# Kernel tuning notes

Hardware: AMD Instinct MI355X
Metric: run time of the kernel (lower is better)

Reference implementation:

```python
import jax, jax.numpy as jnp
import numpy as np


def setup_inputs() -> dict:
    key = jax.random.key(0)
    B, D, KD, TR, NI = 4096, 512, 448, 64, 16  # batch, d_model, key_dim_size, t_resolution, num_iters
    DK = KD + TR                                # full query/key width = 512
    ks = jax.random.split(key, 9)

    def w(k, fan_in, fan_out):
        return jax.random.normal(k, (fan_in, fan_out), jnp.float32) / jnp.sqrt(jnp.float32(fan_in))

    return {
        "x":   jax.random.normal(ks[0], (B, D), jnp.float32),
        "Wik": w(ks[1], D, KD),        # input_key_proj
        "Wiv": w(ks[2], D, D),         # input_value_proj (value dim = d_model)
        "Wq":  w(ks[3], D, DK),        # query_proj
        "Wk":  w(ks[4], D + TR, DK),   # key_proj on concat(block_out, sin(t*t_enc))
        "Wv":  w(ks[5], D, D),         # value_proj
        "W1":  w(ks[6], D, D),         # block MLP layer 1
        "W2":  w(ks[7], D, D),         # block MLP layer 2
        "t_emb": 0.02 * jax.random.normal(ks[8], (NI + 1, D), jnp.float32),  # block time conditioning
    }


def reference(x, Wik, Wiv, Wq, Wk, Wv, W1, W2, t_emb):
    B, D = x.shape
    DK = Wq.shape[1]
    TR = Wk.shape[0] - D           # t_resolution
    NI = t_emb.shape[0] - 1        # num_iters
    dt = x.dtype
    scale = jnp.asarray(1.0 / np.sqrt(DK), dt)
    # t_encoding = pi * (1/2)**i
    t_enc = jnp.pi * (0.5 ** jnp.arange(TR, dtype=dt))

    def attend(q, K, V, n):  # q:[B,DK], K:[B,NI,DK], V:[B,NI,D]; n static valid length
        s = jnp.einsum('bd,btd->bt', q, K[:, :n]) * scale
        p = jax.nn.softmax(s, axis=-1)
        return jnp.einsum('bt,btd->bd', p, V[:, :n])

    def block(A, t):  # opaque self.block(A, t=t): MLP with per-t conditioning
        return jax.nn.gelu(A @ W1 + t_emb[t]) @ W2

    # preallocated growing KV cache (in-place append instead of concat)
    K = jnp.zeros((B, NI, DK), dt)
    V = jnp.zeros((B, NI, D), dt)
    k0 = jnp.pad(x @ Wik, ((0, 0), (0, TR)))  # initial key padded to DK (sin(0)=0 encoding)
    K = K.at[:, 0].set(k0)
    V = V.at[:, 0].set(x @ Wiv)
    q = jnp.ones((B, DK), dt)

    for t in range(NI - 1):  # static unrolled recurrence over iterations
        A = attend(q, K, V, t + 1)
        Bt = block(A, t)
        sin_t = jnp.broadcast_to(jnp.sin(t * t_enc), (B, TR))
        K = K.at[:, t + 1].set(jnp.concatenate([Bt, sin_t], axis=-1) @ Wk)
        V = V.at[:, t + 1].set(Bt @ Wv)
        q = Bt @ Wq

    A = attend(q, K, V, NI)
    return block(A, NI)  # final block call with t = num_iters
```

## Files before the change

kernel.cpp:

```cpp
#include <hip/hip_runtime.h>
#include <hip/hip_bf16.h>
#include <math.h>

typedef unsigned short u16;
using bf16x8 = __attribute__((ext_vector_type(8))) short;
using f32x4  = __attribute__((ext_vector_type(4))) float;

__device__ inline float b2f(u16 u) {
  unsigned v = ((unsigned)u) << 16;
  return __builtin_bit_cast(float, v);
}
__device__ inline u16 f2b(float f) {
  unsigned u = __builtin_bit_cast(unsigned, f);
  u += 0x7fffu + ((u >> 16) & 1u);
  return (u16)(u >> 16);
}
__device__ inline float gelu_f(float x) {
  float x3 = x * x * x;
  return 0.5f * x * (1.f + tanhf(0.7978845608028654f * (x + 0.044715f * x3)));
}
__device__ inline void gload_lds16(const void* g, void* lds) {
  __builtin_amdgcn_global_load_lds((const __attribute__((address_space(1))) void*)g,
                                   (__attribute__((address_space(3))) void*)lds,
                                   16, 0, 0);
}

#define EPI_SPLIT2 0
#define EPI_F32    1
#define EPI_INIT2H 2

template<int EPI>
__global__ __launch_bounds__(256)
void gemm64(const u16* __restrict__ Aptr, int lda,
            const u16* __restrict__ BT,
            void* __restrict__ out0, void* __restrict__ out1, void* __restrict__ out2,
            const u16* __restrict__ fvec, const float* __restrict__ tembv, int t1)
{
  constexpr int BM = 128, BN = 64, WN = 32, NR = 2, MR = 4;
  __shared__ alignas(16) char Ash[3][BM * 128];
  __shared__ alignas(16) char Bsh[3][BN * 128];
  const int tid = threadIdx.x, lane = tid & 63, wid = tid >> 6;
  const int wm = wid >> 1, wn = wid & 1;
  const int bm = blockIdx.x, bn = blockIdx.y;

  const int rIn = lane >> 3;
  const int c16log = (lane & 7) ^ (rIn & 7);

  auto stage = [&](int buf, int kt) {
    #pragma unroll
    for (int i = 0; i < 4; ++i) {
      int c = wid * 4 + i;
      int row = c * 8 + rIn;
      gload_lds16(Aptr + (size_t)(bm * BM + row) * lda + kt + c16log * 8,
                  Ash[buf] + c * 1024);
    }
    #pragma unroll
    for (int i = 0; i < 2; ++i) {
      int c = wid * 2 + i;
      int row = c * 8 + rIn;
      gload_lds16(BT + (size_t)(bn * BN + row) * 512 + kt + c16log * 8,
                  Bsh[buf] + c * 1024);
    }
  };

  f32x4 acc[MR][NR] = {};
  stage(0, 0);
  stage(1, 64);
  #pragma unroll
  for (int kt = 0; kt < 8; ++kt) {
    const int cb = kt % 3;
    if (kt < 6) {
      stage((kt + 2) % 3, (kt + 2) * 64);
      asm volatile("s_waitcnt vmcnt(12)" ::: "memory");
    } else if (kt == 6) {
      asm volatile("s_waitcnt vmcnt(6)" ::: "memory");
    } else {
      asm volatile("s_waitcnt vmcnt(0)" ::: "memory");
    }
    __builtin_amdgcn_s_barrier();
    asm volatile("" ::: "memory");
    #pragma unroll
    for (int kk = 0; kk < 64; kk += 32) {
      bf16x8 af[MR], bfr[NR];
      #pragma unroll
      for (int m = 0; m < MR; ++m) {
        int R = wm * 64 + m * 16 + (lane & 15);
        int c16 = (kk >> 3) + (lane >> 4);
        af[m] = *(const bf16x8*)(Ash[cb] + R * 128 + ((c16 ^ (R & 7)) << 4));
      }
      #pragma unroll
      for (int n = 0; n < NR; ++n) {
        int R = wn * WN + n * 16 + (lane & 15);
        int c16 = (kk >> 3) + (lane >> 4);
        bfr[n] = *(const bf16x8*)(Bsh[cb] + R * 128 + ((c16 ^ (R & 7)) << 4));
      }
      #pragma unroll
      for (int m = 0; m < MR; ++m)
        #pragma unroll
        for (int n = 0; n < NR; ++n)
          acc[m][n] = __builtin_amdgcn_mfma_f32_16x16x32_bf16(af[m], bfr[n], acc[m][n], 0, 0, 0);
    }
    asm volatile("" ::: "memory");
    __builtin_amdgcn_s_barrier();
    asm volatile("" ::: "memory");
  }

  const int row0 = bm * BM + wm * 64;
  const int col0 = bn * BN + wn * WN;
  #pragma unroll
  for (int m = 0; m < MR; ++m) {
    #pragma unroll
    for (int n = 0; n < NR; ++n) {
      #pragma unroll
      for (int i = 0; i < 4; ++i) {
        int row = row0 + m * 16 + (lane >> 4) * 4 + i;
        int col = col0 + n * 16 + (lane & 15);
        float v = acc[m][n][i];
        if constexpr (EPI == EPI_SPLIT2) {
          if (col < 512) {
            ((u16*)out0)[((size_t)row * 16 + t1) * 512 + col] = f2b(v + b2f(fvec[col]));
          } else {
            ((u16*)out1)[((size_t)row * 16 + t1) * 512 + (col - 512)] = f2b(v);
          }
        } else if constexpr (EPI == EPI_INIT2H) {
          if (col < 512) {
            ((u16*)out0)[(size_t)row * 16 * 512 + col] = f2b(v);
          } else {
            ((u16*)out1)[(size_t)row * 16 * 512 + (col - 512)] = f2b(v);
            ((u16*)out2)[(size_t)row * 512 + (col - 512)] =
                f2b(gelu_f(v + tembv[col - 512]));
          }
        } else {
          ((float*)out0)[(size_t)row * 512 + col] = v;
        }
      }
    }
  }
}

struct BatchJobs {
  const u16* A[5];
  const u16* BT[5];
  u16* O[5];
  int M[5];
};

__global__ __launch_bounds__(256)
void gemm_batch(BatchJobs jb)
{
  constexpr int BM = 128, BN = 64, WN = 32, NR = 2, MR = 4;
  const int z = blockIdx.z;
  if ((int)blockIdx.x * BM >= jb.M[z]) return;
  const u16* __restrict__ Aptr = jb.A[z];
  const u16* __restrict__ BT   = jb.BT[z];
  u16* __restrict__ Optr       = jb.O[z];

  __shared__ alignas(16) char Ash[3][BM * 128];
  __shared__ alignas(16) char Bsh[3][BN * 128];
  const int tid = threadIdx.x, lane = tid & 63, wid = tid >> 6;
  const int wm = wid >> 1, wn = wid & 1;
  const int bm = blockIdx.x, bn = blockIdx.y;

  const int rIn = lane >> 3;
  const int c16log = (lane & 7) ^ (rIn & 7);

  auto stage = [&](int buf, int kt) {
    #pragma unroll
    for (int i = 0; i < 4; ++i) {
      int c = wid * 4 + i;
      int row = c * 8 + rIn;
      gload_lds16(Aptr + (size_t)(bm * BM + row) * 512 + kt + c16log * 8,
                  Ash[buf] + c * 1024);
    }
    #pragma unroll
    for (int i = 0; i < 2; ++i) {
      int c = wid * 2 + i;
      int row = c * 8 + rIn;
      gload_lds16(BT + (size_t)(bn * BN + row) * 512 + kt + c16log * 8,
                  Bsh[buf] + c * 1024);
    }
  };

  f32x4 acc[MR][NR] = {};
  stage(0, 0);
  stage(1, 64);
  #pragma unroll
  for (int kt = 0; kt < 8; ++kt) {
    const int cb = kt % 3;
    if (kt < 6) {
      stage((kt + 2) % 3, (kt + 2) * 64);
      asm volatile("s_waitcnt vmcnt(12)" ::: "memory");
    } else if (kt == 6) {
      asm volatile("s_waitcnt vmcnt(6)" ::: "memory");
    } else {
      asm volatile("s_waitcnt vmcnt(0)" ::: "memory");
    }
    __builtin_amdgcn_s_barrier();
    asm volatile("" ::: "memory");
    #pragma unroll
    for (int kk = 0; kk < 64; kk += 32) {
      bf16x8 af[MR], bfr[NR];
      #pragma unroll
      for (int m = 0; m < MR; ++m) {
        int R = wm * 64 + m * 16 + (lane & 15);
        int c16 = (kk >> 3) + (lane >> 4);
        af[m] = *(const bf16x8*)(Ash[cb] + R * 128 + ((c16 ^ (R & 7)) << 4));
      }
      #pragma unroll
      for (int n = 0; n < NR; ++n) {
        int R = wn * WN + n * 16 + (lane & 15);
        int c16 = (kk >> 3) + (lane >> 4);
        bfr[n] = *(const bf16x8*)(Bsh[cb] + R * 128 + ((c16 ^ (R & 7)) << 4));
      }
      #pragma unroll
      for (int m = 0; m < MR; ++m)
        #pragma unroll
        for (int n = 0; n < NR; ++n)
          acc[m][n] = __builtin_amdgcn_mfma_f32_16x16x32_bf16(af[m], bfr[n], acc[m][n], 0, 0, 0);
    }
    asm volatile("" ::: "memory");
    __builtin_amdgcn_s_barrier();
    asm volatile("" ::: "memory");
  }

  const int row0 = bm * BM + wm * 64;
  const int col0 = bn * BN + wn * WN;
  #pragma unroll
  for (int m = 0; m < MR; ++m)
    #pragma unroll
    for (int n = 0; n < NR; ++n)
      #pragma unroll
      for (int i = 0; i < 4; ++i) {
        int row = row0 + m * 16 + (lane >> 4) * 4 + i;
        int col = col0 + n * 16 + (lane & 15);
        Optr[(size_t)row * 512 + col] = f2b(acc[m][n][i]);
      }
}

__global__ __launch_bounds__(256)
void attend_kernel(const u16* __restrict__ qv, const u16* __restrict__ Kc,
                   const u16* __restrict__ VWc, u16* __restrict__ Hout,
                   const float* __restrict__ temb, int n)
{
  const int lane = threadIdx.x & 63;
  const int w = threadIdx.x >> 6;
  const int b = blockIdx.x * 4 + w;
  const float scale = 0.04419417382415922f;
  const size_t base = (size_t)b * 512 + lane * 8;
  bf16x8 q8 = *(const bf16x8*)(qv + base);
  float qf[8];
  #pragma unroll
  for (int j = 0; j < 8; ++j) qf[j] = b2f((u16)q8[j]);
  float s[16];
  float mx = -1e30f;
  #pragma unroll
  for (int t = 0; t < 16; ++t) {
    if (t < n) {
      bf16x8 k8 = *(const bf16x8*)(Kc + ((size_t)b * 16 + t) * 512 + lane * 8);
      float d = 0.f;
      #pragma unroll
      for (int j = 0; j < 8; ++j) d += qf[j] * b2f((u16)k8[j]);
      #pragma unroll
      for (int off = 32; off > 0; off >>= 1) d += __shfl_xor(d, off, 64);
      s[t] = d * scale;
      mx = fmaxf(mx, s[t]);
    }
  }
  float p[16], sum = 0.f;
  #pragma unroll
  for (int t = 0; t < 16; ++t) if (t < n) { p[t] = expf(s[t] - mx); sum += p[t]; }
  const float inv = 1.f / sum;
  float a[8] = {};
  #pragma unroll
  for (int t = 0; t < 16; ++t) {
    if (t < n) {
      bf16x8 v8 = *(const bf16x8*)(VWc + ((size_t)b * 16 + t) * 512 + lane * 8);
      float pt = p[t] * inv;
      #pragma unroll
      for (int j = 0; j < 8; ++j) a[j] += pt * b2f((u16)v8[j]);
    }
  }
  bf16x8 o;
  #pragma unroll
  for (int j = 0; j < 8; ++j)
    o[j] = (short)f2b(gelu_f(a[j] + temb[lane * 8 + j]));
  *(bf16x8*)(Hout + base) = o;
}

__global__ __launch_bounds__(256)
void prep_kernel(const float* __restrict__ x,   const float* __restrict__ Wik,
                 const float* __restrict__ Wiv, const float* __restrict__ Wq,
                 const float* __restrict__ Wk,  const float* __restrict__ Wv,
                 const float* __restrict__ W1,  const float* __restrict__ W2,
                 u16* __restrict__ W1T, u16* __restrict__ W2T, u16* __restrict__ WqT,
                 u16* __restrict__ WkT, u16* __restrict__ WvT,
                 u16* __restrict__ W2b, u16* __restrict__ Wivb, u16* __restrict__ xb,
                 u16* __restrict__ Wikpadb, u16* __restrict__ biasKpad)
{
  const int bid = blockIdx.x, tid = threadIdx.x;
  if (bid < 1280) {
    __shared__ float tile[32][33];
    const int mat = bid >> 8, local = bid & 255;
    const float* in = (mat == 0) ? W1 : (mat == 1) ? W2 : (mat == 2) ? Wq
                    : (mat == 3) ? Wk : Wv;
    u16* out = (mat == 0) ? W1T : (mat == 1) ? W2T : (mat == 2) ? WqT
             : (mat == 3) ? WkT : WvT;
    const int tx = tid & 31, ty = tid >> 5;
    const int c0 = (local & 15) * 32, r0 = (local >> 4) * 32;
    #pragma unroll
    for (int rr = 0; rr < 32; rr += 8)
      tile[ty + rr][tx] = in[(size_t)(r0 + ty + rr) * 512 + c0 + tx];
    __syncthreads();
    #pragma unroll
    for (int rr = 0; rr < 32; rr += 8)
      out[(size_t)(c0 + ty + rr) * 512 + r0 + tx] = f2b(tile[tx][ty + rr]);
  } else if (bid < 3840) {
    const float* in; u16* out; int local;
    if (bid < 1536)      { in = W2;  out = W2b;  local = bid - 1280; }
    else if (bid < 1792) { in = Wiv; out = Wivb; local = bid - 1536; }
    else                 { in = x;   out = xb;   local = bid - 1792; }
    const int i = local * 256 + tid;
    const float4 v = ((const float4*)in)[i];
    ushort4 o;
    o.x = f2b(v.x); o.y = f2b(v.y); o.z = f2b(v.z); o.w = f2b(v.w);
    ((ushort4*)out)[i] = o;
  } else if (bid < 4096) {
    const int local = bid - 3840;
    const int e = local * 1024 + tid * 4;
    const int r = e >> 9, c0 = e & 511;
    ushort4 o;
    float v0 = (c0 + 0 < 448) ? Wik[(size_t)r * 448 + c0 + 0] : 0.f;
    float v1 = (c0 + 1 < 448) ? Wik[(size_t)r * 448 + c0 + 1] : 0.f;
    float v2 = (c0 + 2 < 448) ? Wik[(size_t)r * 448 + c0 + 2] : 0.f;
    float v3 = (c0 + 3 < 448) ? Wik[(size_t)r * 448 + c0 + 3] : 0.f;
    o.x = f2b(v0); o.y = f2b(v1); o.z = f2b(v2); o.w = f2b(v3);
    *(ushort4*)(Wikpadb + (size_t)r * 512 + c0) = o;
  } else {
    const int local = bid - 4096;
    const int t = local >> 1;
    const int col = ((local & 1) << 8) + tid;
    float acc = 0.f;
    if (t < 15) {
      #pragma unroll
      for (int r = 0; r < 64; ++r) {
        float tenc = 3.14159265358979323846f * exp2f(-(float)r);
        acc += sinf((float)t * tenc) * Wk[(size_t)(512 + r) * 512 + col];
      }
    }
    biasKpad[(size_t)t * 512 + col] = f2b(acc);
  }
}

extern "C" void kernel_launch(void* const* d_in, const int* in_sizes, int n_in,
                              void* d_out, int out_size, void* d_ws, size_t ws_size,
                              hipStream_t stream)
{
  const float* x    = (const float*)d_in[0];
  const float* Wik  = (const float*)d_in[1];
  const float* Wiv  = (const float*)d_in[2];
  const float* Wq   = (const float*)d_in[3];
  const float* Wk   = (const float*)d_in[4];
  const float* Wv   = (const float*)d_in[5];
  const float* W1   = (const float*)d_in[6];
  const float* W2   = (const float*)d_in[7];
  const float* temb = (const float*)d_in[8];

  char* ws = (char*)d_ws;
  size_t off = 0;
  auto alloc = [&](size_t bytes) {
    char* p = ws + off;
    off += (bytes + 255) & ~(size_t)255;
    return p;
  };
  const size_t SQ = (size_t)512 * 512 * 2;
  u16* W1T     = (u16*)alloc(SQ);
  u16* W2T     = (u16*)alloc(SQ);
  u16* WqT     = (u16*)alloc(SQ);
  u16* WkT     = (u16*)alloc(SQ);
  u16* WvT     = (u16*)alloc(SQ);
  u16* W2b     = (u16*)alloc(SQ);
  u16* Wivb    = (u16*)alloc(SQ);
  u16* Wikpadb = (u16*)alloc(SQ);
  u16* biasKpad= (u16*)alloc((size_t)128 * 512 * 2);
  u16* W2Wq    = (u16*)alloc(SQ);
  u16* W2WkD   = (u16*)alloc(SQ);
  u16* W2Wv    = (u16*)alloc(SQ);
  u16* biasC   = (u16*)alloc((size_t)128 * 512 * 2);
  u16* PT2     = (u16*)alloc((size_t)1024 * 512 * 2);
  u16* ITn     = (u16*)alloc((size_t)1024 * 512 * 2);
  u16* xb      = (u16*)alloc((size_t)4096 * 512 * 2);
  u16* Kc      = (u16*)alloc((size_t)4096 * 16 * 512 * 2);
  u16* VWc     = (u16*)alloc((size_t)4096 * 16 * 512 * 2);
  u16* Hb      = (u16*)alloc((size_t)4096 * 512 * 2);

  dim3 blk(256);
  prep_kernel<<<dim3(4352), blk, 0, stream>>>(
      x, Wik, Wiv, Wq, Wk, Wv, W1, W2,
      W1T, W2T, WqT, WkT, WvT, W2b, Wivb, xb, Wikpadb, biasKpad);

  BatchJobs b1 = {};
  b1.A[0] = W2b; b1.BT[0] = WqT; b1.O[0] = W2Wq;  b1.M[0] = 512;
  b1.A[1] = W2b; b1.BT[1] = WkT; b1.O[1] = W2WkD; b1.M[1] = 512;
  b1.A[2] = W2b; b1.BT[2] = WvT; b1.O[2] = W2Wv;  b1.M[2] = 512;
  gemm_batch<<<dim3(4, 8, 3), blk, 0, stream>>>(b1);

  BatchJobs b2 = {};
  b2.A[0] = W2Wq;     b2.BT[0] = W2WkD;   b2.O[0] = PT2;                       b2.M[0] = 512;
  b2.A[1] = W1T;      b2.BT[1] = W2Wv;    b2.O[1] = PT2 + (size_t)512 * 512;   b2.M[1] = 512;
  b2.A[2] = W2Wq;     b2.BT[2] = Wikpadb; b2.O[2] = ITn;                       b2.M[2] = 512;
  b2.A[3] = W1T;      b2.BT[3] = Wivb;    b2.O[3] = ITn + (size_t)512 * 512;   b2.M[3] = 512;
  b2.A[4] = biasKpad; b2.BT[4] = W2Wq;    b2.O[4] = biasC;                     b2.M[4] = 128;
  gemm_batch<<<dim3(4, 8, 5), blk, 0, stream>>>(b2);

  gemm64<EPI_INIT2H><<<dim3(32, 16), blk, 0, stream>>>(
      xb, 512, ITn, Kc, VWc, Hb, nullptr, temb, 0);

  for (int t = 0; t < 15; ++t) {
    gemm64<EPI_SPLIT2><<<dim3(32, 16), blk, 0, stream>>>(
        Hb, 512, PT2, Kc, VWc, nullptr, biasC + (size_t)t * 512, nullptr, t + 1);
    const int ti = (t == 14) ? 16 : t + 1;
    attend_kernel<<<dim3(1024), blk, 0, stream>>>(
        Hb, Kc, VWc, Hb, temb + (size_t)ti * 512, t + 2);
  }
  gemm64<EPI_F32><<<dim3(32, 8), blk, 0, stream>>>(
      Hb, 512, W2T, d_out, nullptr, nullptr, nullptr, nullptr, 0);
}
```

Measured before the change: 518.7 us.

## Fuse recurrence into one persistent kernel with per-block rows held in LDS

Replaces the 32 per-iteration GEMM and attention launches with a single persistent kernel. Each block owns 16 batch rows, keeps its H tile in LDS, and alternates a GEMM phase and an attention phase separated by block barriers, so no kernel relaunches and no global H round-trips are needed. The GEMM phase reads the weight matrix directly from global/L2 into registers for every block without LDS reuse. That greatly raises cache traffic and leaves only one 4-wave block per CU, which trades launch and sync overhead for lower data reuse and occupancy.

```diff
diff --git a/kernel.cpp b/kernel.cpp
--- a/kernel.cpp
+++ b/kernel.cpp
@@ -25,18 +25,166 @@
                                    16, 0, 0);
 }
 
-#define EPI_SPLIT2 0
-#define EPI_F32    1
-#define EPI_INIT2H 2
-
-template<int EPI>
+
+template<int COLS, int F32OUT>
+__device__ __forceinline__ void gemm_phase(
+    const u16* Hs, const u16* __restrict__ BT, const u16* __restrict__ bias,
+    u16* __restrict__ Kc, u16* __restrict__ VWc, float* __restrict__ outp,
+    int r0, int slot, int lane, int wid)
+{
+  bf16x8 areg[16];
+  {
+    const int r = lane & 15, hi = lane >> 4;
+    #pragma unroll
+    for (int kk = 0; kk < 16; ++kk) {
+      const int c16 = (kk * 4 + hi) ^ (r & 7);
+      areg[kk] = *(const bf16x8*)((const char*)Hs + r * 1024 + c16 * 16);
+    }
+  }
+  constexpr int NCT = COLS / 64;
+  const int colb = wid * (COLS / 4);
+  const int rowb = (lane >> 4) * 4;
+  const int hi = lane >> 4;
+
+  auto loadB = [&](bf16x8* dst, int ct) {
+    const u16* base = BT + (size_t)(colb + ct * 16 + (lane & 15)) * 512 + hi * 8;
+    #pragma unroll
+    for (int kk = 0; kk < 16; ++kk)
+      dst[kk] = *(const bf16x8*)(base + kk * 32);
+  };
+  auto epi = [&](int ct, const f32x4& a) {
+    #pragma unroll
+    for (int i = 0; i < 4; ++i) {
+      const int g = colb + ct * 16 + (lane & 15);
+      const int row = r0 + rowb + i;
+      const float v = a[i];
+      if constexpr (F32OUT) {
+        outp[(size_t)row * 512 + g] = v;
+      } else {
+        if (g < 512) {
+          Kc[((size_t)row * 16 + slot) * 512 + g] = f2b(v + b2f(bias[g]));
+        } else {
+          VWc[((size_t)row * 16 + slot) * 512 + (g - 512)] = f2b(v);
+        }
+      }
+    }
+  };
+
+  bf16x8 b0[16], b1[16];
+  #pragma unroll
+  for (int cp = 0; cp < NCT / 2; ++cp) {
+    loadB(b0, 2 * cp);
+    loadB(b1, 2 * cp + 1);
+    f32x4 a0 = {0.f, 0.f, 0.f, 0.f}, a1 = {0.f, 0.f, 0.f, 0.f};
+    #pragma unroll
+    for (int kk = 0; kk < 16; ++kk) {
+      a0 = __builtin_amdgcn_mfma_f32_16x16x32_bf16(areg[kk], b0[kk], a0, 0, 0, 0);
+      a1 = __builtin_amdgcn_mfma_f32_16x16x32_bf16(areg[kk], b1[kk], a1, 0, 0, 0);
+    }
+    epi(2 * cp, a0);
+    epi(2 * cp + 1, a1);
+  }
+}
+
+__global__ __launch_bounds__(256, 1)
+void persist_kernel(const u16* __restrict__ xb,
+                    const u16* __restrict__ ITn, const u16* __restrict__ PT2,
+                    const u16* __restrict__ W2T, const u16* __restrict__ biasC,
+                    const float* __restrict__ temb,
+                    u16* __restrict__ Kc, u16* __restrict__ VWc,
+                    float* __restrict__ outp)
+{
+  __shared__ alignas(16) u16 Hs[16 * 512];
+  const int tid = threadIdx.x, lane = tid & 63, wid = tid >> 6;
+  const int r0 = blockIdx.x * 16;
+  const float scale = 0.04419417382415922f;
+
+  #pragma unroll
+  for (int p = 0; p < 4; ++p) {
+    const int s16 = (p * 4 + wid) * 64 + lane;
+    const int r = s16 >> 6, c16 = s16 & 63;
+    gload_lds16(xb + (size_t)(r0 + r) * 512 + (size_t)(c16 ^ (r & 7)) * 8,
+                (char*)Hs + (size_t)(p * 4 + wid) * 1024);
+  }
+  asm volatile("s_waitcnt vmcnt(0)" ::: "memory");
+  __syncthreads();
+
+  for (int t = -1; t < 15; ++t) {
+    gemm_phase<1024, 0>(Hs, (t == -1) ? ITn : PT2,
+                        biasC + (size_t)((t == -1) ? 15 : t) * 512,
+                        Kc, VWc, nullptr, r0, t + 1, lane, wid);
+    __syncthreads();
+
+    const int n = t + 2;
+    const float* tv = temb + (size_t)((t == 14) ? 16 : t + 1) * 512;
+    for (int rr = 0; rr < 4; ++rr) {
+      const int r = wid * 4 + rr;
+      const bf16x8 q8 = *(const bf16x8*)((const char*)Hs + r * 1024 +
+                                         ((lane ^ (r & 7)) << 4));
+      float qf[8];
+      #pragma unroll
+      for (int j = 0; j < 8; ++j) qf[j] = b2f((u16)q8[j]);
+      const u16* kbase = Kc + ((size_t)(r0 + r) * 16) * 512 + lane * 8;
+      const u16* vbase = VWc + ((size_t)(r0 + r) * 16) * 512 + lane * 8;
+      float s[16];
+      float mx = -1e30f;
+      #pragma unroll
+      for (int j = 0; j < 16; ++j) {
+        if (j < n) {
+          const bf16x8 k8 = *(const bf16x8*)(kbase + j * 512);
+          float d = 0.f;
+          #pragma unroll
+          for (int e = 0; e < 8; ++e) d += qf[e] * b2f((u16)k8[e]);
+          #pragma unroll
+          for (int off = 32; off > 0; off >>= 1) d += __shfl_xor(d, off, 64);
+          s[j] = d * scale;
+          mx = fmaxf(mx, s[j]);
+        }
+      }
+      float p[16], sum = 0.f;
+      #pragma unroll
+      for (int j = 0; j < 16; ++j)
+        if (j < n) { p[j] = expf(s[j] - mx); sum += p[j]; }
+      const float inv = 1.f / sum;
+      float a[8] = {};
+      #pragma unroll
+      for (int j = 0; j < 16; ++j) {
+        if (j < n) {
+          const bf16x8 v8 = *(const bf16x8*)(vbase + j * 512);
+          const float pj = p[j] * inv;
+          #pragma unroll
+          for (int e = 0; e < 8; ++e) a[e] += pj * b2f((u16)v8[e]);
+        }
+      }
+      bf16x8 o;
+      #pragma unroll
+      for (int e = 0; e < 8; ++e)
+        o[e] = (short)f2b(gelu_f(a[e] + tv[lane * 8 + e]));
+      *(bf16x8*)((char*)Hs + r * 1024 + ((lane ^ (r & 7)) << 4)) = o;
+    }
+    __syncthreads();
+  }
+
+  gemm_phase<512, 1>(Hs, W2T, nullptr, nullptr, nullptr, outp, r0, 0, lane, wid);
+}
+
+struct BatchJobs {
+  const u16* A[5];
+  const u16* BT[5];
+  u16* O[5];
+  int M[5];
+};
+
 __global__ __launch_bounds__(256)
-void gemm64(const u16* __restrict__ Aptr, int lda,
-            const u16* __restrict__ BT,
-            void* __restrict__ out0, void* __restrict__ out1, void* __restrict__ out2,
-            const u16* __restrict__ fvec, const float* __restrict__ tembv, int t1)
+void gemm_batch(BatchJobs jb)
 {
   constexpr int BM = 128, BN = 64, WN = 32, NR = 2, MR = 4;
+  const int z = blockIdx.z;
+  if ((int)blockIdx.x * BM >= jb.M[z]) return;
+  const u16* __restrict__ Aptr = jb.A[z];
+  const u16* __restrict__ BT   = jb.BT[z];
+  u16* __restrict__ Optr       = jb.O[z];
+
   __shared__ alignas(16) char Ash[3][BM * 128];
   __shared__ alignas(16) char Bsh[3][BN * 128];
   const int tid = threadIdx.x, lane = tid & 63, wid = tid >> 6;
@@ -51,7 +199,7 @@
     for (int i = 0; i < 4; ++i) {
       int c = wid * 4 + i;
       int row = c * 8 + rIn;
-      gload_lds16(Aptr + (size_t)(bm * BM + row) * lda + kt + c16log * 8,
+      gload_lds16(Aptr + (size_t)(bm * BM + row) * 512 + kt + c16log * 8,
                   Ash[buf] + c * 1024);
     }
     #pragma unroll
@@ -108,124 +256,6 @@
   const int row0 = bm * BM + wm * 64;
   const int col0 = bn * BN + wn * WN;
   #pragma unroll
-  for (int m = 0; m < MR; ++m) {
-    #pragma unroll
-    for (int n = 0; n < NR; ++n) {
-      #pragma unroll
-      for (int i = 0; i < 4; ++i) {
-        int row = row0 + m * 16 + (lane >> 4) * 4 + i;
-        int col = col0 + n * 16 + (lane & 15);
-        float v = acc[m][n][i];
-        if constexpr (EPI == EPI_SPLIT2) {
-          if (col < 512) {
-            ((u16*)out0)[((size_t)row * 16 + t1) * 512 + col] = f2b(v + b2f(fvec[col]));
-          } else {
-            ((u16*)out1)[((size_t)row * 16 + t1) * 512 + (col - 512)] = f2b(v);
-          }
-        } else if constexpr (EPI == EPI_INIT2H) {
-          if (col < 512) {
-            ((u16*)out0)[(size_t)row * 16 * 512 + col] = f2b(v);
-          } else {
-            ((u16*)out1)[(size_t)row * 16 * 512 + (col - 512)] = f2b(v);
-            ((u16*)out2)[(size_t)row * 512 + (col - 512)] =
-                f2b(gelu_f(v + tembv[col - 512]));
-          }
-        } else {
-          ((float*)out0)[(size_t)row * 512 + col] = v;
-        }
-      }
-    }
-  }
-}
-
-struct BatchJobs {
-  const u16* A[5];
-  const u16* BT[5];
-  u16* O[5];
-  int M[5];
-};
-
-__global__ __launch_bounds__(256)
-void gemm_batch(BatchJobs jb)
-{
-  constexpr int BM = 128, BN = 64, WN = 32, NR = 2, MR = 4;
-  const int z = blockIdx.z;
-  if ((int)blockIdx.x * BM >= jb.M[z]) return;
-  const u16* __restrict__ Aptr = jb.A[z];
-  const u16* __restrict__ BT   = jb.BT[z];
-  u16* __restrict__ Optr       = jb.O[z];
-
-  __shared__ alignas(16) char Ash[3][BM * 128];
-  __shared__ alignas(16) char Bsh[3][BN * 128];
-  const int tid = threadIdx.x, lane = tid & 63, wid = tid >> 6;
-  const int wm = wid >> 1, wn = wid & 1;
-  const int bm = blockIdx.x, bn = blockIdx.y;
-
-  const int rIn = lane >> 3;
-  const int c16log = (lane & 7) ^ (rIn & 7);
-
-  auto stage = [&](int buf, int kt) {
-    #pragma unroll
-    for (int i = 0; i < 4; ++i) {
-      int c = wid * 4 + i;
-      int row = c * 8 + rIn;
-      gload_lds16(Aptr + (size_t)(bm * BM + row) * 512 + kt + c16log * 8,
-                  Ash[buf] + c * 1024);
-    }
-    #pragma unroll
-    for (int i = 0; i < 2; ++i) {
-      int c = wid * 2 + i;
-      int row = c * 8 + rIn;
-      gload_lds16(BT + (size_t)(bn * BN + row) * 512 + kt + c16log * 8,
-                  Bsh[buf] + c * 1024);
-    }
-  };
-
-  f32x4 acc[MR][NR] = {};
-  stage(0, 0);
-  stage(1, 64);
-  #pragma unroll
-  for (int kt = 0; kt < 8; ++kt) {
-    const int cb = kt % 3;
-    if (kt < 6) {
-      stage((kt + 2) % 3, (kt + 2) * 64);
-      asm volatile("s_waitcnt vmcnt(12)" ::: "memory");
-    } else if (kt == 6) {
-      asm volatile("s_waitcnt vmcnt(6)" ::: "memory");
-    } else {
-      asm volatile("s_waitcnt vmcnt(0)" ::: "memory");
-    }
-    __builtin_amdgcn_s_barrier();
-    asm volatile("" ::: "memory");
-    #pragma unroll
-    for (int kk = 0; kk < 64; kk += 32) {
-      bf16x8 af[MR], bfr[NR];
-      #pragma unroll
-      for (int m = 0; m < MR; ++m) {
-        int R = wm * 64 + m * 16 + (lane & 15);
-        int c16 = (kk >> 3) + (lane >> 4);
-        af[m] = *(const bf16x8*)(Ash[cb] + R * 128 + ((c16 ^ (R & 7)) << 4));
-      }
-      #pragma unroll
-      for (int n = 0; n < NR; ++n) {
-        int R = wn * WN + n * 16 + (lane & 15);
-        int c16 = (kk >> 3) + (lane >> 4);
-        bfr[n] = *(const bf16x8*)(Bsh[cb] + R * 128 + ((c16 ^ (R & 7)) << 4));
-      }
-      #pragma unroll
-      for (int m = 0; m < MR; ++m)
-        #pragma unroll
-        for (int n = 0; n < NR; ++n)
-          acc[m][n] = __builtin_amdgcn_mfma_f32_16x16x32_bf16(af[m], bfr[n], acc[m][n], 0, 0, 0);
-    }
-    asm volatile("" ::: "memory");
-    __builtin_amdgcn_s_barrier();
-    asm volatile("" ::: "memory");
-  }
-
-  const int row0 = bm * BM + wm * 64;
-  const int col0 = bn * BN + wn * WN;
-  #pragma unroll
   for (int m = 0; m < MR; ++m)
     #pragma unroll
     for (int n = 0; n < NR; ++n)
@@ -235,56 +265,6 @@
         int col = col0 + n * 16 + (lane & 15);
         Optr[(size_t)row * 512 + col] = f2b(acc[m][n][i]);
       }
-}
-
-__global__ __launch_bounds__(256)
-void attend_kernel(const u16* __restrict__ qv, const u16* __restrict__ Kc,
-                   const u16* __restrict__ VWc, u16* __restrict__ Hout,
-                   const float* __restrict__ temb, int n)
-{
-  const int lane = threadIdx.x & 63;
-  const int w = threadIdx.x >> 6;
-  const int b = blockIdx.x * 4 + w;
-  const float scale = 0.04419417382415922f;
-  const size_t base = (size_t)b * 512 + lane * 8;
-  bf16x8 q8 = *(const bf16x8*)(qv + base);
-  float qf[8];
-  #pragma unroll
-  for (int j = 0; j < 8; ++j) qf[j] = b2f((u16)q8[j]);
-  float s[16];
-  float mx = -1e30f;
-  #pragma unroll
-  for (int t = 0; t < 16; ++t) {
-    if (t < n) {
-      bf16x8 k8 = *(const bf16x8*)(Kc + ((size_t)b * 16 + t) * 512 + lane * 8);
-      float d = 0.f;
-      #pragma unroll
-      for (int j = 0; j < 8; ++j) d += qf[j] * b2f((u16)k8[j]);
-      #pragma unroll
-      for (int off = 32; off > 0; off >>= 1) d += __shfl_xor(d, off, 64);
-      s[t] = d * scale;
-      mx = fmaxf(mx, s[t]);
-    }
-  }
-  float p[16], sum = 0.f;
-  #pragma unroll
-  for (int t = 0; t < 16; ++t) if (t < n) { p[t] = expf(s[t] - mx); sum += p[t]; }
-  const float inv = 1.f / sum;
-  float a[8] = {};
-  #pragma unroll
-  for (int t = 0; t < 16; ++t) {
-    if (t < n) {
-      bf16x8 v8 = *(const bf16x8*)(VWc + ((size_t)b * 16 + t) * 512 + lane * 8);
-      float pt = p[t] * inv;
-      #pragma unroll
-      for (int j = 0; j < 8; ++j) a[j] += pt * b2f((u16)v8[j]);
-    }
-  }
-  bf16x8 o;
-  #pragma unroll
-  for (int j = 0; j < 8; ++j)
-    o[j] = (short)f2b(gelu_f(a[j] + temb[lane * 8 + j]));
-  *(bf16x8*)(Hout + base) = o;
 }
 
 __global__ __launch_bounds__(256)
@@ -391,7 +371,6 @@
   u16* xb      = (u16*)alloc((size_t)4096 * 512 * 2);
   u16* Kc      = (u16*)alloc((size_t)4096 * 16 * 512 * 2);
   u16* VWc     = (u16*)alloc((size_t)4096 * 16 * 512 * 2);
-  u16* Hb      = (u16*)alloc((size_t)4096 * 512 * 2);
 
   dim3 blk(256);
   prep_kernel<<<dim3(4352), blk, 0, stream>>>(
@@ -412,16 +391,6 @@
   b2.A[4] = biasKpad; b2.BT[4] = W2Wq;    b2.O[4] = biasC;                     b2.M[4] = 128;
   gemm_batch<<<dim3(4, 8, 5), blk, 0, stream>>>(b2);
 
-  gemm64<EPI_INIT2H><<<dim3(32, 16), blk, 0, stream>>>(
-      xb, 512, ITn, Kc, VWc, Hb, nullptr, temb, 0);
-
-  for (int t = 0; t < 15; ++t) {
-    gemm64<EPI_SPLIT2><<<dim3(32, 16), blk, 0, stream>>>(
-        Hb, 512, PT2, Kc, VWc, nullptr, biasC + (size_t)t * 512, nullptr, t + 1);
-    const int ti = (t == 14) ? 16 : t + 1;
-    attend_kernel<<<dim3(1024), blk, 0, stream>>>(
-        Hb, Kc, VWc, Hb, temb + (size_t)ti * 512, t + 2);
-  }
-  gemm64<EPI_F32><<<dim3(32, 8), blk, 0, stream>>>(
-      Hb, 512, W2T, d_out, nullptr, nullptr, nullptr, nullptr, 0);
-}
+  persist_kernel<<<dim3(256), blk, 0, stream>>>(
+      xb, ITn, PT2, W2T, biasC, temb, Kc, VWc, (float*)d_out);
+}
```

Result: slower. 1.130 ms (+117.9%).

## Fuse recurrence into one persistent cooperative kernel with grid barriers

Applied to the files above, without the earlier changes.

Replaces the 32 separate launches (initial GEMM, 15 GEMM+attend pairs, final GEMM) with a single cooperative persistent kernel of 512 blocks. Software grid barriers built on atomics separate the GEMM and attention phases. The initial step now reuses the split GEMM epilogue and a length-1 attention in place of the special init epilogue. The aim is to remove per-launch overhead and tail gaps between kernels. In exchange it adds barrier spin costs and depends on two blocks fitting per CU, and it falls back to the old launch sequence if the cooperative launch fails.

```diff
diff --git a/kernel.cpp b/kernel.cpp
--- a/kernel.cpp
+++ b/kernel.cpp
@@ -30,19 +30,15 @@
 #define EPI_INIT2H 2
 
 template<int EPI>
-__global__ __launch_bounds__(256)
-void gemm64(const u16* __restrict__ Aptr, int lda,
-            const u16* __restrict__ BT,
-            void* __restrict__ out0, void* __restrict__ out1, void* __restrict__ out2,
-            const u16* __restrict__ fvec, const float* __restrict__ tembv, int t1)
-{
-  constexpr int BM = 128, BN = 64, WN = 32, NR = 2, MR = 4;
-  __shared__ alignas(16) char Ash[3][BM * 128];
-  __shared__ alignas(16) char Bsh[3][BN * 128];
-  const int tid = threadIdx.x, lane = tid & 63, wid = tid >> 6;
+__device__ __forceinline__ void gemm_dev(
+    char* AshB, char* BshB,
+    const u16* __restrict__ Aptr, int lda, const u16* __restrict__ BT,
+    void* __restrict__ out0, void* __restrict__ out1, void* __restrict__ out2,
+    const u16* __restrict__ fvec, const float* __restrict__ tembv,
+    int t1, int bm, int bn, int lane, int wid)
+{
+  constexpr int WN = 32, NR = 2, MR = 4;
   const int wm = wid >> 1, wn = wid & 1;
-  const int bm = blockIdx.x, bn = blockIdx.y;
-
   const int rIn = lane >> 3;
   const int c16log = (lane & 7) ^ (rIn & 7);
 
@@ -51,15 +47,15 @@
     for (int i = 0; i < 4; ++i) {
       int c = wid * 4 + i;
       int row = c * 8 + rIn;
-      gload_lds16(Aptr + (size_t)(bm * BM + row) * lda + kt + c16log * 8,
-                  Ash[buf] + c * 1024);
+      gload_lds16(Aptr + (size_t)(bm * 128 + row) * lda + kt + c16log * 8,
+                  AshB + buf * 16384 + c * 1024);
     }
     #pragma unroll
     for (int i = 0; i < 2; ++i) {
       int c = wid * 2 + i;
       int row = c * 8 + rIn;
-      gload_lds16(BT + (size_t)(bn * BN + row) * 512 + kt + c16log * 8,
-                  Bsh[buf] + c * 1024);
+      gload_lds16(BT + (size_t)(bn * 64 + row) * 512 + kt + c16log * 8,
+                  BshB + buf * 8192 + c * 1024);
     }
   };
 
@@ -86,13 +82,13 @@
       for (int m = 0; m < MR; ++m) {
         int R = wm * 64 + m * 16 + (lane & 15);
         int c16 = (kk >> 3) + (lane >> 4);
-        af[m] = *(const bf16x8*)(Ash[cb] + R * 128 + ((c16 ^ (R & 7)) << 4));
+        af[m] = *(const bf16x8*)(AshB + cb * 16384 + R * 128 + ((c16 ^ (R & 7)) << 4));
       }
       #pragma unroll
       for (int n = 0; n < NR; ++n) {
         int R = wn * WN + n * 16 + (lane & 15);
         int c16 = (kk >> 3) + (lane >> 4);
-        bfr[n] = *(const bf16x8*)(Bsh[cb] + R * 128 + ((c16 ^ (R & 7)) << 4));
+        bfr[n] = *(const bf16x8*)(BshB + cb * 8192 + R * 128 + ((c16 ^ (R & 7)) << 4));
       }
       #pragma unroll
       for (int m = 0; m < MR; ++m)
@@ -105,8 +101,8 @@
     asm volatile("" ::: "memory");
   }
 
-  const int row0 = bm * BM + wm * 64;
-  const int col0 = bn * BN + wn * WN;
+  const int row0 = bm * 128 + wm * 64;
+  const int col0 = bn * 64 + wn * WN;
   #pragma unroll
   for (int m = 0; m < MR; ++m) {
     #pragma unroll
@@ -138,6 +134,127 @@
   }
 }
 
+template<int EPI>
+__global__ __launch_bounds__(256)
+void gemm64(const u16* __restrict__ Aptr, int lda,
+            const u16* __restrict__ BT,
+            void* __restrict__ out0, void* __restrict__ out1, void* __restrict__ out2,
+            const u16* __restrict__ fvec, const float* __restrict__ tembv, int t1)
+{
+  __shared__ alignas(16) char Ash[3 * 16384];
+  __shared__ alignas(16) char Bsh[3 * 8192];
+  gemm_dev<EPI>(Ash, Bsh, Aptr, lda, BT, out0, out1, out2, fvec, tembv, t1,
+                blockIdx.x, blockIdx.y, threadIdx.x & 63, threadIdx.x >> 6);
+}
+
+__device__ __forceinline__ void attend_row(
+    const u16* __restrict__ Hq, const u16* __restrict__ Kc,
+    const u16* __restrict__ VWc, u16* __restrict__ Hout,
+    const float* __restrict__ tv, int n, int r, int lane)
+{
+  const float scale = 0.04419417382415922f;
+  const size_t base = (size_t)r * 512 + lane * 8;
+  bf16x8 q8 = *(const bf16x8*)(Hq + base);
+  float qf[8];
+  #pragma unroll
+  for (int j = 0; j < 8; ++j) qf[j] = b2f((u16)q8[j]);
+  const u16* kbase = Kc + ((size_t)r * 16) * 512 + lane * 8;
+  const u16* vbase = VWc + ((size_t)r * 16) * 512 + lane * 8;
+  float s[16];
+  float mx = -1e30f;
+  #pragma unroll
+  for (int j = 0; j < 16; ++j) {
+    if (j < n) {
+      const bf16x8 k8 = *(const bf16x8*)(kbase + j * 512);
+      float d = 0.f;
+      #pragma unroll
+      for (int e = 0; e < 8; ++e) d += qf[e] * b2f((u16)k8[e]);
+      #pragma unroll
+      for (int off = 32; off > 0; off >>= 1) d += __shfl_xor(d, off, 64);
+      s[j] = d * scale;
+      mx = fmaxf(mx, s[j]);
+    }
+  }
+  float p[16], sum = 0.f;
+  #pragma unroll
+  for (int j = 0; j < 16; ++j)
+    if (j < n) { p[j] = expf(s[j] - mx); sum += p[j]; }
+  const float inv = 1.f / sum;
+  float a[8] = {};
+  #pragma unroll
+  for (int j = 0; j < 16; ++j) {
+    if (j < n) {
+      const bf16x8 v8 = *(const bf16x8*)(vbase + j * 512);
+      const float pj = p[j] * inv;
+      #pragma unroll
+      for (int e = 0; e < 8; ++e) a[e] += pj * b2f((u16)v8[e]);
+    }
+  }
+  bf16x8 o;
+  #pragma unroll
+  for (int e = 0; e < 8; ++e)
+    o[e] = (short)f2b(gelu_f(a[e] + tv[lane * 8 + e]));
+  *(bf16x8*)(Hout + base) = o;
+}
+
+__global__ __launch_bounds__(256)
+void attend_kernel(const u16* __restrict__ qv, const u16* __restrict__ Kc,
+                   const u16* __restrict__ VWc, u16* __restrict__ Hout,
+                   const float* __restrict__ temb, int n)
+{
+  const int lane = threadIdx.x & 63;
+  const int r = blockIdx.x * 4 + (threadIdx.x >> 6);
+  attend_row(qv, Kc, VWc, Hout, temb, n, r, lane);
+}
+
+__device__ __forceinline__ void gridbar(unsigned* bar, unsigned target) {
+  __syncthreads();
+  if (threadIdx.x == 0) {
+    __hip_atomic_fetch_add(bar, 1u, __ATOMIC_RELEASE, __HIP_MEMORY_SCOPE_AGENT);
+    while (__hip_atomic_load(bar, __ATOMIC_RELAXED, __HIP_MEMORY_SCOPE_AGENT) < target)
+      __builtin_amdgcn_s_sleep(8);
+    (void)__hip_atomic_load(bar, __ATOMIC_ACQUIRE, __HIP_MEMORY_SCOPE_AGENT);
+  }
+  __syncthreads();
+}
+
+__global__ __launch_bounds__(256, 2)
+void persist_kernel(const u16* __restrict__ xb,
+                    const u16* __restrict__ ITn, const u16* __restrict__ PT2,
+                    const u16* __restrict__ W2T, const u16* __restrict__ biasC,
+                    const float* __restrict__ temb,
+                    u16* __restrict__ Kc, u16* __restrict__ VWc,
+                    u16* __restrict__ Hb, float* __restrict__ outp,
+                    unsigned* __restrict__ bar)
+{
+  __shared__ alignas(16) char Ash[3 * 16384];
+  __shared__ alignas(16) char Bsh[3 * 8192];
+  const int tid = threadIdx.x, lane = tid & 63, wid = tid >> 6;
+  const int bid = blockIdx.x;
+  unsigned phase = 0;
+
+  for (int t = -1; t < 15; ++t) {
+    gemm_dev<EPI_SPLIT2>(Ash, Bsh,
+                         (t == -1) ? xb : Hb, 512,
+                         (t == -1) ? ITn : PT2,
+                         Kc, VWc, nullptr,
+                         biasC + (size_t)((t == -1) ? 15 : t) * 512, nullptr,
+                         t + 1, bid >> 4, bid & 15, lane, wid);
+    gridbar(bar, 512u * (++phase));
+
+    const int n = t + 2;
+    const float* tv = temb + (size_t)((t == 14) ? 16 : t + 1) * 512;
+    #pragma unroll
+    for (int rr = 0; rr < 2; ++rr)
+      attend_row(Hb, Kc, VWc, Hb, tv, n, bid * 8 + wid * 2 + rr, lane);
+    gridbar(bar, 512u * (++phase));
+  }
+
+  if (bid < 256)
+    gemm_dev<EPI_F32>(Ash, Bsh, Hb, 512, W2T, outp, nullptr, nullptr,
+                      nullptr, nullptr, 0, bid >> 3, bid & 7, lane, wid);
+}
+
 struct BatchJobs {
   const u16* A[5];
   const u16* BT[5];
@@ -148,19 +265,16 @@
 __global__ __launch_bounds__(256)
 void gemm_batch(BatchJobs jb)
 {
-  constexpr int BM = 128, BN = 64, WN = 32, NR = 2, MR = 4;
   const int z = blockIdx.z;
-  if ((int)blockIdx.x * BM >= jb.M[z]) return;
-  const u16* __restrict__ Aptr = jb.A[z];
-  const u16* __restrict__ BT   = jb.BT[z];
-  u16* __restrict__ Optr       = jb.O[z];
-
-  __shared__ alignas(16) char Ash[3][BM * 128];
-  __shared__ alignas(16) char Bsh[3][BN * 128];
+  if ((int)blockIdx.x * 128 >= jb.M[z]) return;
+  __shared__ alignas(16) char Ash[3 * 16384];
+  __shared__ alignas(16) char Bsh[3 * 8192];
+  const u16* A = jb.A[z];
+  const u16* BT = jb.BT[z];
+  u16* O = jb.O[z];
   const int tid = threadIdx.x, lane = tid & 63, wid = tid >> 6;
   const int wm = wid >> 1, wn = wid & 1;
   const int bm = blockIdx.x, bn = blockIdx.y;
-
   const int rIn = lane >> 3;
   const int c16log = (lane & 7) ^ (rIn & 7);
 
@@ -169,19 +283,19 @@
     for (int i = 0; i < 4; ++i) {
       int c = wid * 4 + i;
       int row = c * 8 + rIn;
-      gload_lds16(Aptr + (size_t)(bm * BM + row) * 512 + kt + c16log * 8,
-                  Ash[buf] + c * 1024);
+      gload_lds16(A + (size_t)(bm * 128 + row) * 512 + kt + c16log * 8,
+                  Ash + buf * 16384 + c * 1024);
     }
     #pragma unroll
     for (int i = 0; i < 2; ++i) {
       int c = wid * 2 + i;
       int row = c * 8 + rIn;
-      gload_lds16(BT + (size_t)(bn * BN + row) * 512 + kt + c16log * 8,
-                  Bsh[buf] + c * 1024);
+      gload_lds16(BT + (size_t)(bn * 64 + row) * 512 + kt + c16log * 8,
+                  Bsh + buf * 8192 + c * 1024);
     }
   };
 
-  f32x4 acc[MR][NR] = {};
+  f32x4 acc[4][2] = {};
   stage(0, 0);
   stage(1, 64);
   #pragma unroll
@@ -199,23 +313,23 @@
     asm volatile("" ::: "memory");
     #pragma unroll
     for (int kk = 0; kk < 64; kk += 32) {
-      bf16x8 af[MR], bfr[NR];
-      #pragma unroll
-      for (int m = 0; m < MR; ++m) {
+      bf16x8 af[4], bfr[2];
+      #pragma unroll
+      for (int m = 0; m < 4; ++m) {
         int R = wm * 64 + m * 16 + (lane & 15);
         int c16 = (kk >> 3) + (lane >> 4);
-        af[m] = *(const bf16x8*)(Ash[cb] + R * 128 + ((c16 ^ (R & 7)) << 4));
-      }
-      #pragma unroll
-      for (int n = 0; n < NR; ++n) {
-        int R = wn * WN + n * 16 + (lane & 15);
+        af[m] = *(const bf16x8*)(Ash + cb * 16384 + R * 128 + ((c16 ^ (R & 7)) << 4));
+      }
+      #pragma unroll
+      for (int n = 0; n < 2; ++n) {
+        int R = wn * 32 + n * 16 + (lane & 15);
         int c16 = (kk >> 3) + (lane >> 4);
-        bfr[n] = *(const bf16x8*)(Bsh[cb] + R * 128 + ((c16 ^ (R & 7)) << 4));
-      }
-      #pragma unroll
-      for (int m = 0; m < MR; ++m)
+        bfr[n] = *(const bf16x8*)(Bsh + cb * 8192 + R * 128 + ((c16 ^ (R & 7)) << 4));
+      }
+      #pragma unroll
+      for (int m = 0; m < 4; ++m)
         #pragma unroll
-        for (int n = 0; n < NR; ++n)
+        for (int n = 0; n < 2; ++n)
           acc[m][n] = __builtin_amdgcn_mfma_f32_16x16x32_bf16(af[m], bfr[n], acc[m][n], 0, 0, 0);
     }
     asm volatile("" ::: "memory");
@@ -223,68 +337,18 @@
     asm volatile("" ::: "memory");
   }
 
-  const int row0 = bm * BM + wm * 64;
-  const int col0 = bn * BN + wn * WN;
-  #pragma unroll
-  for (int m = 0; m < MR; ++m)
-    #pragma unroll
-    for (int n = 0; n < NR; ++n)
+  const int row0 = bm * 128 + wm * 64;
+  const int col0 = bn * 64 + wn * 32;
+  #pragma unroll
+  for (int m = 0; m < 4; ++m)
+    #pragma unroll
+    for (int n = 0; n < 2; ++n)
       #pragma unroll
       for (int i = 0; i < 4; ++i) {
         int row = row0 + m * 16 + (lane >> 4) * 4 + i;
         int col = col0 + n * 16 + (lane & 15);
-        Optr[(size_t)row * 512 + col] = f2b(acc[m][n][i]);
-      }
-}
-
-__global__ __launch_bounds__(256)
-void attend_kernel(const u16* __restrict__ qv, const u16* __restrict__ Kc,
-                   const u16* __restrict__ VWc, u16* __restrict__ Hout,
-                   const float* __restrict__ temb, int n)
-{
-  const int lane = threadIdx.x & 63;
-  const int w = threadIdx.x >> 6;
-  const int b = blockIdx.x * 4 + w;
-  const float scale = 0.04419417382415922f;
-  const size_t base = (size_t)b * 512 + lane * 8;
-  bf16x8 q8 = *(const bf16x8*)(qv + base);
-  float qf[8];
-  #pragma unroll
-  for (int j = 0; j < 8; ++j) qf[j] = b2f((u16)q8[j]);
-  float s[16];
-  float mx = -1e30f;
-  #pragma unroll
-  for (int t = 0; t < 16; ++t) {
-    if (t < n) {
-      bf16x8 k8 = *(const bf16x8*)(Kc + ((size_t)b * 16 + t) * 512 + lane * 8);
-      float d = 0.f;
-      #pragma unroll
-      for (int j = 0; j < 8; ++j) d += qf[j] * b2f((u16)k8[j]);
-      #pragma unroll
-      for (int off = 32; off > 0; off >>= 1) d += __shfl_xor(d, off, 64);
-      s[t] = d * scale;
-      mx = fmaxf(mx, s[t]);
-    }
-  }
-  float p[16], sum = 0.f;
-  #pragma unroll
-  for (int t = 0; t < 16; ++t) if (t < n) { p[t] = expf(s[t] - mx); sum += p[t]; }
-  const float inv = 1.f / sum;
-  float a[8] = {};
-  #pragma unroll
-  for (int t = 0; t < 16; ++t) {
-    if (t < n) {
-      bf16x8 v8 = *(const bf16x8*)(VWc + ((size_t)b * 16 + t) * 512 + lane * 8);
-      float pt = p[t] * inv;
-      #pragma unroll
-      for (int j = 0; j < 8; ++j) a[j] += pt * b2f((u16)v8[j]);
-    }
-  }
-  bf16x8 o;
-  #pragma unroll
-  for (int j = 0; j < 8; ++j)
-    o[j] = (short)f2b(gelu_f(a[j] + temb[lane * 8 + j]));
-  *(bf16x8*)(Hout + base) = o;
+        O[(size_t)row * 512 + col] = f2b(acc[m][n][i]);
+      }
 }
 
 __global__ __launch_bounds__(256)
@@ -295,9 +359,11 @@
                  u16* __restrict__ W1T, u16* __restrict__ W2T, u16* __restrict__ WqT,
                  u16* __restrict__ WkT, u16* __restrict__ WvT,
                  u16* __restrict__ W2b, u16* __restrict__ Wivb, u16* __restrict__ xb,
-                 u16* __restrict__ Wikpadb, u16* __restrict__ biasKpad)
+                 u16* __restrict__ Wikpadb, u16* __restrict__ biasKpad,
+                 unsigned* __restrict__ bar)
 {
   const int bid = blockIdx.x, tid = threadIdx.x;
+  if (bid == 0 && tid == 0) *bar = 0u;
   if (bid < 1280) {
     __shared__ float tile[32][33];
     const int mat = bid >> 8, local = bid & 255;
@@ -392,11 +458,12 @@
   u16* Kc      = (u16*)alloc((size_t)4096 * 16 * 512 * 2);
   u16* VWc     = (u16*)alloc((size_t)4096 * 16 * 512 * 2);
   u16* Hb      = (u16*)alloc((size_t)4096 * 512 * 2);
+  unsigned* bar= (unsigned*)alloc(256);
 
   dim3 blk(256);
   prep_kernel<<<dim3(4352), blk, 0, stream>>>(
       x, Wik, Wiv, Wq, Wk, Wv, W1, W2,
-      W1T, W2T, WqT, WkT, WvT, W2b, Wivb, xb, Wikpadb, biasKpad);
+      W1T, W2T, WqT, WkT, WvT, W2b, Wivb, xb, Wikpadb, biasKpad, bar);
 
   BatchJobs b1 = {};
   b1.A[0] = W2b; b1.BT[0] = WqT; b1.O[0] = W2Wq;  b1.M[0] = 512;
@@ -412,16 +479,27 @@
   b2.A[4] = biasKpad; b2.BT[4] = W2Wq;    b2.O[4] = biasC;                     b2.M[4] = 128;
   gemm_batch<<<dim3(4, 8, 5), blk, 0, stream>>>(b2);
 
-  gemm64<EPI_INIT2H><<<dim3(32, 16), blk, 0, stream>>>(
-      xb, 512, ITn, Kc, VWc, Hb, nullptr, temb, 0);
-
-  for (int t = 0; t < 15; ++t) {
-    gemm64<EPI_SPLIT2><<<dim3(32, 16), blk, 0, stream>>>(
-        Hb, 512, PT2, Kc, VWc, nullptr, biasC + (size_t)t * 512, nullptr, t + 1);
-    const int ti = (t == 14) ? 16 : t + 1;
-    attend_kernel<<<dim3(1024), blk, 0, stream>>>(
-        Hb, Kc, VWc, Hb, temb + (size_t)ti * 512, t + 2);
-  }
-  gemm64<EPI_F32><<<dim3(32, 8), blk, 0, stream>>>(
-      Hb, 512, W2T, d_out, nullptr, nullptr, nullptr, nullptr, 0);
-}
+  const u16* xb_c = xb;  const u16* ITn_c = ITn;  const u16* PT2_c = PT2;
+  const u16* W2T_c = W2T; const u16* biasC_c = biasC; const float* temb_c = temb;
+  float* outp = (float*)d_out;
+  void* pargs[] = {
+    (void*)&xb_c, (void*)&ITn_c, (void*)&PT2_c, (void*)&W2T_c, (void*)&biasC_c,
+    (void*)&temb_c, (void*)&Kc, (void*)&VWc, (void*)&Hb, (void*)&outp,
+    (void*)&bar};
+  hipError_t rc = hipLaunchCooperativeKernel(
+      (const void*)persist_kernel, dim3(512), blk, pargs, 0, stream);
+
+  if (rc != hipSuccess) {
+    gemm64<EPI_INIT2H><<<dim3(32, 16), blk, 0, stream>>>(
+        xb, 512, ITn, Kc, VWc, Hb, nullptr, temb, 0);
+    for (int t = 0; t < 15; ++t) {
+      gemm64<EPI_SPLIT2><<<dim3(32, 16), blk, 0, stream>>>(
+          Hb, 512, PT2, Kc, VWc, nullptr, biasC + (size_t)t * 512, nullptr, t + 1);
+      const int ti = (t == 14) ? 16 : t + 1;
+      attend_kernel<<<dim3(1024), blk, 0, stream>>>(
+          Hb, Kc, VWc, Hb, temb + (size_t)ti * 512, t + 2);
+    }
+    gemm64<EPI_F32><<<dim3(32, 8), blk, 0, stream>>>(
+        Hb, 512, W2T, d_out, nullptr, nullptr, nullptr, nullptr, 0);
+  }
+}
```

Measured after the change: 1.987 ms. 283% more time.
